# Kernel tuning notes

Measured on AMD Instinct MI355X. Metric: run time of the kernel, lower is better.

Reference implementation:

```python
import jax, jax.numpy as jnp
import numpy as np

TEAM = 5
N_PLAYER = 131072
PD = 256
HD = 256
MLP_H = 512
B = 16384

def _combine(t=TEAM):
    i1, i2 = [], []
    for i in range(t):
        for j in range(t):
            if i != j:
                i1.append(i); i2.append(j)
    return np.array(i1), np.array(i2)

IDX1, IDX2 = _combine()

def setup_inputs() -> dict:
    key = jax.random.key(0)
    ks = jax.random.split(key, 12)
    def xavier(k, shape):
        fan_in, fan_out = shape[1], shape[0]
        std = np.sqrt(2.0 / (fan_in + fan_out))
        return (jax.random.normal(k, shape, dtype=jnp.float32) * std)
    return {
        'team_ids': jax.random.randint(ks[0], (B, TEAM), 0, N_PLAYER),
        'emb': xavier(ks[1], (N_PLAYER, PD)),
        'fm_w1': xavier(ks[2], (2 * HD, PD)),
        'fm_b1': jnp.zeros((2 * HD,), jnp.float32),
        'fm_w2': xavier(ks[3], (HD, 2 * HD)),
        'fm_b2': jnp.zeros((HD,), jnp.float32),
        'att_w': xavier(ks[4], (HD, HD)),
        'att_b': jnp.zeros((HD,), jnp.float32),
        'mlp_w1': xavier(ks[5], (MLP_H, HD)),
        'mlp_b1': jnp.zeros((MLP_H,), jnp.float32),
        'mlp_w2': xavier(ks[6], (1, MLP_H)),
        'mlp_b2': jnp.zeros((1,), jnp.float32),
    }

def reference(team_ids, emb, fm_w1, fm_b1, fm_w2, fm_b2, att_w, att_b,
              mlp_w1, mlp_b1, mlp_w2, mlp_b2):
    # embedding lookup: [B, 5, PD]
    x = emb[team_ids]
    # feature mapper: Linear -> SiLU -> Linear  => [B, 5, HD]
    h = jax.nn.silu(jnp.einsum('btp,hp->bth', x, fm_w1) + fm_b1)
    h = jnp.einsum('bth,oh->bto', h, fm_w2) + fm_b2
    # pairwise gather (20 ordered pairs): [B, 20, HD]
    a = h[:, IDX1]
    b = h[:, IDX2]
    prod = a * b
    # small MLP (dropout is inference identity): [B, 20]
    m = jax.nn.silu(jnp.einsum('bph,mh->bpm', prod, mlp_w1) + mlp_b1)
    order2 = (jnp.einsum('bpm,om->bpo', m, mlp_w2) + mlp_b2)[..., 0]
    # attention (reduce=True -> view [B, 5, 4, HD], softmax over axis 2)
    wa = jnp.einsum('bph,oh->bpo', a, att_w) + att_b
    score = (wa * b).sum(-1).reshape(-1, TEAM, TEAM - 1)
    normal = jax.nn.softmax(score, axis=2).reshape(-1, TEAM * (TEAM - 1))
    order2 = order2 * normal
    return order2.sum(axis=1, keepdims=True)  # [B, 1]
```

## Files before the change

### kernel.cpp

```cpp
#include <hip/hip_runtime.h>

#define NB     16384
#define TEAM   5
#define NPAIR  20
#define UPAIR  10
#define PD     256
#define HD     256
#define H1D    512
#define NPLAY  (NB*TEAM)
#define NCHUNK 1

typedef __attribute__((ext_vector_type(4))) float f32x4;
typedef __attribute__((ext_vector_type(8))) short s16x8;

__device__ __forceinline__ float silu_f(float x){ return x / (1.0f + __expf(-x)); }

__device__ __forceinline__ unsigned short bf16_rne(float x){
  unsigned u = __float_as_uint(x);
  unsigned r = u + 0x7fffu + ((u >> 16) & 1u);
  return (unsigned short)(r >> 16);
}
__device__ __forceinline__ float bf16_to_f(unsigned short s){
  return __uint_as_float(((unsigned)s) << 16);
}
__device__ __forceinline__ void tsplit(float x, short& h, short& l){
  const unsigned u = __float_as_uint(x);
  h = (short)(u >> 16);
  const float lf = x - __uint_as_float(u & 0xffff0000u);
  l = (short)(__float_as_uint(lf) >> 16);
}

__global__ void k_pack(const float* __restrict__ w, short* __restrict__ wf,
                       int KT, int total)
{
  const int tid = blockIdx.x * 256 + threadIdx.x;
  if (tid >= total) return;
  const int slot = tid & 7;
  const int lane = (tid >> 3) & 63;
  const int grp  = tid >> 9;
  const int kt   = grp % KT;
  const int nt   = grp / KT;
  const int K    = KT * 32;
  const int n = nt * 16 + (lane & 15);
  const int k = kt * 32 + ((lane >> 4) << 3) + slot;
  const float v = w[(size_t)n * K + k];
  const unsigned short hi = bf16_rne(v);
  const float lo = v - bf16_to_f(hi);
  wf[tid]         = (short)hi;
  wf[total + tid] = (short)bf16_rne(lo);
}

__global__ __launch_bounds__(256) void k_l1(
    const int* __restrict__ tids, const float* __restrict__ emb,
    const short* __restrict__ w1f, const float* __restrict__ b1,
    float* __restrict__ Hh1)
{
  __shared__ short Af[10240];
  __shared__ float Bb[256];
  __shared__ int   Tid[80];

  const int t = threadIdx.x, lane = t & 63, w = t >> 6;
  const int bx = blockIdx.x, cy = blockIdx.y;
  const int p0 = bx * 80;

  if (t < 80) Tid[t] = tids[p0 + t];
  Bb[t] = b1[cy * 256 + t];

  f32x4 acc[5][4];
  #pragma unroll
  for (int mt = 0; mt < 5; ++mt)
    #pragma unroll
    for (int j = 0; j < 4; ++j) acc[mt][j] = (f32x4){0.f,0.f,0.f,0.f};

  const s16x8* Bh = reinterpret_cast<const s16x8*>(w1f);

  for (int kt = 0; kt < 8; ++kt) {
    const int kc = kt >> 1, ks = kt & 1;
    if (ks == 0) {
      __syncthreads();
      const int kt0 = kc * 64;
      #pragma unroll
      for (int f = 0; f < 5; ++f) {
        const int idx4  = t + f * 256;
        const int sg    = (idx4 & 1) * 4;
        const int lane_ = (idx4 >> 1) & 63;
        const int ks_   = (idx4 >> 7) & 1;
        const int mt_   = idx4 >> 8;
        const int p     = mt_ * 16 + (lane_ & 15);
        const int k     = kt0 + ks_ * 32 + ((lane_ >> 4) << 3) + sg;
        const int row   = Tid[p];
        const float4 a4 = *reinterpret_cast<const float4*>(emb + (size_t)row * PD + k);
        float pv[4] = {a4.x, a4.y, a4.z, a4.w};
        short hi[4], lo[4];
        #pragma unroll
        for (int e = 0; e < 4; ++e) tsplit(pv[e], hi[e], lo[e]);
        const int aoff = (mt_ * 2 + ks_) * 512 + lane_ * 8 + sg;
        *reinterpret_cast<short4*>(&Af[aoff])        = make_short4(hi[0],hi[1],hi[2],hi[3]);
        *reinterpret_cast<short4*>(&Af[5120 + aoff]) = make_short4(lo[0],lo[1],lo[2],lo[3]);
      }
      __syncthreads();
    }

    s16x8 ah[5], al[5];
    #pragma unroll
    for (int mt = 0; mt < 5; ++mt) {
      ah[mt] = *reinterpret_cast<const s16x8*>(&Af[(mt*2 + ks)*512 + lane*8]);
      al[mt] = *reinterpret_cast<const s16x8*>(&Af[5120 + (mt*2 + ks)*512 + lane*8]);
    }
    #pragma unroll
    for (int j = 0; j < 4; ++j) {
      const int nt = cy * 16 + w * 4 + j;
      const s16x8 bh = Bh[(nt*8 + kt)*64 + lane];
      const s16x8 bl = Bh[16384 + (nt*8 + kt)*64 + lane];
      #pragma unroll
      for (int mt = 0; mt < 5; ++mt) {
        acc[mt][j] = __builtin_amdgcn_mfma_f32_16x16x32_bf16(ah[mt], bh, acc[mt][j], 0,0,0);
        acc[mt][j] = __builtin_amdgcn_mfma_f32_16x16x32_bf16(al[mt], bh, acc[mt][j], 0,0,0);
        acc[mt][j] = __builtin_amdgcn_mfma_f32_16x16x32_bf16(ah[mt], bl, acc[mt][j], 0,0,0);
      }
    }
  }

  #pragma unroll
  for (int mt = 0; mt < 5; ++mt)
    #pragma unroll
    for (int j = 0; j < 4; ++j) {
      const int nl = w * 64 + j * 16 + (lane & 15);
      const int n  = cy * 256 + nl;
      #pragma unroll
      for (int r = 0; r < 4; ++r) {
        const int p = p0 + mt*16 + ((lane >> 4) << 2) + r;
        Hh1[(size_t)p * H1D + n] = silu_f(acc[mt][j][r] + Bb[nl]);
      }
    }
}

__global__ __launch_bounds__(256) void k_l2(
    const float* __restrict__ Hh1, const short* __restrict__ w2f,
    const float* __restrict__ b2, float* __restrict__ Hout)
{
  __shared__ short Af[10240];
  __shared__ float Bb[256];

  const int t = threadIdx.x, lane = t & 63, w = t >> 6;
  const int bx = blockIdx.x;
  const int p0 = bx * 80;

  Bb[t] = b2[t];

  const int sg    = (t & 1) * 4;
  const int lane_ = (t >> 1) & 63;
  const int ks_   = (t >> 7) & 1;
  const int kb    = ks_ * 32 + ((lane_ >> 4) << 3) + sg;
  int rowH[5], aof[5];
  #pragma unroll
  for (int f = 0; f < 5; ++f) {
    rowH[f] = (p0 + f * 16 + (lane_ & 15)) * H1D;
    aof[f]  = (f * 2 + ks_) * 512 + lane_ * 8 + sg;
  }

  f32x4 acc[5][4];
  #pragma unroll
  for (int mt = 0; mt < 5; ++mt)
    #pragma unroll
    for (int j = 0; j < 4; ++j) acc[mt][j] = (f32x4){0.f,0.f,0.f,0.f};

  const s16x8* B2 = reinterpret_cast<const s16x8*>(w2f);

  for (int kt = 0; kt < 16; ++kt) {
    const int kc = kt >> 1, ks = kt & 1;
    if (ks == 0) {
      __syncthreads();
      const int kk = kc * 64 + kb;
      #pragma unroll
      for (int f = 0; f < 5; ++f) {
        const float4 a4 = *reinterpret_cast<const float4*>(Hh1 + rowH[f] + kk);
        float pv[4] = {a4.x, a4.y, a4.z, a4.w};
        short hi[4], lo[4];
        #pragma unroll
        for (int e = 0; e < 4; ++e) tsplit(pv[e], hi[e], lo[e]);
        *reinterpret_cast<short4*>(&Af[aof[f]])        = make_short4(hi[0],hi[1],hi[2],hi[3]);
        *reinterpret_cast<short4*>(&Af[5120 + aof[f]]) = make_short4(lo[0],lo[1],lo[2],lo[3]);
      }
      __syncthreads();
    }

    s16x8 ah[5], al[5];
    #pragma unroll
    for (int mt = 0; mt < 5; ++mt) {
      ah[mt] = *reinterpret_cast<const s16x8*>(&Af[(mt*2 + ks)*512 + lane*8]);
      al[mt] = *reinterpret_cast<const s16x8*>(&Af[5120 + (mt*2 + ks)*512 + lane*8]);
    }
    #pragma unroll
    for (int j = 0; j < 4; ++j) {
      const int nt = w * 4 + j;
      const s16x8 bh = B2[(nt*16 + kt)*64 + lane];
      const s16x8 bl = B2[16384 + (nt*16 + kt)*64 + lane];
      #pragma unroll
      for (int mt = 0; mt < 5; ++mt) {
        acc[mt][j] = __builtin_amdgcn_mfma_f32_16x16x32_bf16(ah[mt], bh, acc[mt][j], 0,0,0);
        acc[mt][j] = __builtin_amdgcn_mfma_f32_16x16x32_bf16(al[mt], bh, acc[mt][j], 0,0,0);
        acc[mt][j] = __builtin_amdgcn_mfma_f32_16x16x32_bf16(ah[mt], bl, acc[mt][j], 0,0,0);
      }
    }
  }

  #pragma unroll
  for (int mt = 0; mt < 5; ++mt)
    #pragma unroll
    for (int j = 0; j < 4; ++j) {
      const int n = w * 64 + j * 16 + (lane & 15);
      #pragma unroll
      for (int r = 0; r < 4; ++r) {
        const int p = p0 + mt*16 + ((lane >> 4) << 2) + r;
        Hout[(size_t)p * PD + n] = acc[mt][j][r] + Bb[n];
      }
    }
}

__global__ __launch_bounds__(256) void k_fm4(
    const int* __restrict__ tids, const float* __restrict__ emb,
    const short* __restrict__ w1f, const float* __restrict__ b1,
    const short* __restrict__ w2f, const float* __restrict__ b2,
    float* __restrict__ Hout)
{
  __shared__ char smem[65536 + 3072];
  short* Af  = reinterpret_cast<short*>(smem);
  short* H1f = reinterpret_cast<short*>(smem);
  float* Bb  = reinterpret_cast<float*>(smem + 65536);

  const int t = threadIdx.x, lane = t & 63, w = t >> 6;
  const int m0 = blockIdx.x * 32;

  Bb[t]       = b1[t];
  Bb[t + 256] = b1[t + 256];
  Bb[t + 512] = b2[t];

  #pragma unroll
  for (int f = 0; f < 8; ++f) {
    const int g     = t + f * 256;
    const int sg    = (g & 1) * 4;
    const int lane_ = (g >> 1) & 63;
    const int kt_   = (g >> 7) & 7;
    const int mt_   = g >> 10;
    const int p     = mt_ * 16 + (lane_ & 15);
    const int k     = kt_ * 32 + ((lane_ >> 4) << 3) + sg;
    const int row   = tids[m0 + p];
    const float4 a4 = *reinterpret_cast<const float4*>(emb + (size_t)row * PD + k);
    float pv[4] = {a4.x, a4.y, a4.z, a4.w};
    short hi[4], lo[4];
    #pragma unroll
    for (int e = 0; e < 4; ++e) {
      const unsigned short h = bf16_rne(pv[e]);
      hi[e] = (short)h;
      lo[e] = (short)bf16_rne(pv[e] - bf16_to_f(h));
    }
    const int off = ((mt_*8 + kt_)*64 + lane_)*8 + sg;
    *reinterpret_cast<short4*>(&Af[off])        = make_short4(hi[0],hi[1],hi[2],hi[3]);
    *reinterpret_cast<short4*>(&Af[8192 + off]) = make_short4(lo[0],lo[1],lo[2],lo[3]);
  }
  __syncthreads();

  const s16x8* B1 = reinterpret_cast<const s16x8*>(w1f);
  const s16x8* B2 = reinterpret_cast<const s16x8*>(w2f);

  f32x4 acc1[2][8];
  #pragma unroll
  for (int mt = 0; mt < 2; ++mt)
    #pragma unroll
    for (int j = 0; j < 8; ++j) acc1[mt][j] = (f32x4){0.f,0.f,0.f,0.f};

  #pragma unroll
  for (int kt = 0; kt < 8; ++kt) {
    s16x8 ah[2], al[2];
    #pragma unroll
    for (int mt = 0; mt < 2; ++mt) {
      ah[mt] = *reinterpret_cast<const s16x8*>(&Af[((mt*8 + kt)*64 + lane)*8]);
      al[mt] = *reinterpret_cast<const s16x8*>(&Af[8192 + ((mt*8 + kt)*64 + lane)*8]);
    }
    #pragma unroll
    for (int j = 0; j < 8; ++j) {
      const int nt = w * 8 + j;
      const s16x8 bh = B1[(nt*8 + kt)*64 + lane];
      const s16x8 bl = B1[16384 + (nt*8 + kt)*64 + lane];
      #pragma unroll
      for (int mt = 0; mt < 2; ++mt) {
        acc1[mt][j] = __builtin_amdgcn_mfma_f32_16x16x32_bf16(ah[mt], bh, acc1[mt][j], 0,0,0);
        acc1[mt][j] = __builtin_amdgcn_mfma_f32_16x16x32_bf16(al[mt], bh, acc1[mt][j], 0,0,0);
        acc1[mt][j] = __builtin_amdgcn_mfma_f32_16x16x32_bf16(ah[mt], bl, acc1[mt][j], 0,0,0);
      }
    }
  }
  __syncthreads();

  #pragma unroll
  for (int mt = 0; mt < 2; ++mt)
    #pragma unroll
    for (int j = 0; j < 8; ++j) {
      const int n     = w * 128 + j * 16 + (lane & 15);
      const int kt2   = n >> 5;
      const int lhalf = 16 * ((n >> 3) & 3);
      const int slot2 = n & 7;
      #pragma unroll
      for (int r = 0; r < 4; ++r) {
        const int prow = ((lane >> 4) << 2) + r;
        const float v = silu_f(acc1[mt][j][r] + Bb[n]);
        const unsigned short hi = bf16_rne(v);
        const int off = ((mt*16 + kt2)*64 + lhalf + prow)*8 + slot2;
        H1f[off]         = (short)hi;
        H1f[16384 + off] = (short)bf16_rne(v - bf16_to_f(hi));
      }
    }
  __syncthreads();

  f32x4 acc2[2][4];
  #pragma unroll
  for (int mt = 0; mt < 2; ++mt)
    #pragma unroll
    for (int j = 0; j < 4; ++j) acc2[mt][j] = (f32x4){0.f,0.f,0.f,0.f};

  #pragma unroll
  for (int kt = 0; kt < 16; ++kt) {
    s16x8 ah[2], al[2];
    #pragma unroll
    for (int mt = 0; mt < 2; ++mt) {
      ah[mt] = *reinterpret_cast<const s16x8*>(&H1f[((mt*16 + kt)*64 + lane)*8]);
      al[mt] = *reinterpret_cast<const s16x8*>(&H1f[16384 + ((mt*16 + kt)*64 + lane)*8]);
    }
    #pragma unroll
    for (int j = 0; j < 4; ++j) {
      const int nt = w * 4 + j;
      const s16x8 bh = B2[(nt*16 + kt)*64 + lane];
      const s16x8 bl = B2[16384 + (nt*16 + kt)*64 + lane];
      #pragma unroll
      for (int mt = 0; mt < 2; ++mt) {
        acc2[mt][j] = __builtin_amdgcn_mfma_f32_16x16x32_bf16(ah[mt], bh, acc2[mt][j], 0,0,0);
        acc2[mt][j] = __builtin_amdgcn_mfma_f32_16x16x32_bf16(al[mt], bh, acc2[mt][j], 0,0,0);
        acc2[mt][j] = __builtin_amdgcn_mfma_f32_16x16x32_bf16(ah[mt], bl, acc2[mt][j], 0,0,0);
      }
    }
  }

  #pragma unroll
  for (int mt = 0; mt < 2; ++mt)
    #pragma unroll
    for (int j = 0; j < 4; ++j) {
      const int n = w * 64 + j * 16 + (lane & 15);
      #pragma unroll
      for (int r = 0; r < 4; ++r) {
        const int p = m0 + mt*16 + ((lane >> 4) << 2) + r;
        Hout[(size_t)p * PD + n] = acc2[mt][j][r] + Bb[512 + n];
      }
    }
}

__global__ __launch_bounds__(256) void k_score(
    const float* __restrict__ Hin, const short* __restrict__ attf,
    const float* __restrict__ attb, float* __restrict__ SC)
{
  __shared__ char smem[49152 + 1024];
  short* Hf  = reinterpret_cast<short*>(smem);
  float* WAl = reinterpret_cast<float*>(smem);
  float* Ab  = reinterpret_cast<float*>(smem + 49152);

  const int t = threadIdx.x, lane = t & 63, w = t >> 6;
  const int b0 = blockIdx.x * 8;
  const float* src = Hin + (size_t)b0 * TEAM * PD;

  Ab[t] = attb[t];

  #pragma unroll
  for (int f = 0; f < 12; ++f) {
    const int g     = t + f * 256;
    const int sg    = (g & 1) * 4;
    const int lane_ = (g >> 1) & 63;
    const int kt_   = (g >> 7) & 7;
    const int mt_   = g >> 10;
    const int p     = mt_ * 16 + (lane_ & 15);
    const int k     = kt_ * 32 + ((lane_ >> 4) << 3) + sg;
    float4 a4 = make_float4(0.f, 0.f, 0.f, 0.f);
    if (p < 40) a4 = *reinterpret_cast<const float4*>(src + (size_t)p * PD + k);
    float pv[4] = {a4.x, a4.y, a4.z, a4.w};
    short hi[4], lo[4];
    #pragma unroll
    for (int e = 0; e < 4; ++e) tsplit(pv[e], hi[e], lo[e]);
    const int off = ((mt_*8 + kt_)*64 + lane_)*8 + sg;
    *reinterpret_cast<short4*>(&Hf[off])         = make_short4(hi[0],hi[1],hi[2],hi[3]);
    *reinterpret_cast<short4*>(&Hf[12288 + off]) = make_short4(lo[0],lo[1],lo[2],lo[3]);
  }
  __syncthreads();

  f32x4 acc[3][4];
  #pragma unroll
  for (int mt = 0; mt < 3; ++mt)
    #pragma unroll
    for (int j = 0; j < 4; ++j) acc[mt][j] = (f32x4){0.f,0.f,0.f,0.f};

  const s16x8* Bh = reinterpret_cast<const s16x8*>(attf);
  #pragma unroll
  for (int kt = 0; kt < 8; ++kt) {
    s16x8 ah[3], al[3];
    #pragma unroll
    for (int mt = 0; mt < 3; ++mt) {
      ah[mt] = *reinterpret_cast<const s16x8*>(&Hf[((mt*8 + kt)*64 + lane)*8]);
      al[mt] = *reinterpret_cast<const s16x8*>(&Hf[12288 + ((mt*8 + kt)*64 + lane)*8]);
    }
    #pragma unroll
    for (int j = 0; j < 4; ++j) {
      const int nt = w * 4 + j;
      const s16x8 bh = Bh[(nt*8 + kt)*64 + lane];
      const s16x8 bl = Bh[8192 + (nt*8 + kt)*64 + lane];
      #pragma unroll
      for (int mt = 0; mt < 3; ++mt) {
        acc[mt][j] = __builtin_amdgcn_mfma_f32_16x16x32_bf16(ah[mt], bh, acc[mt][j], 0,0,0);
        acc[mt][j] = __builtin_amdgcn_mfma_f32_16x16x32_bf16(al[mt], bh, acc[mt][j], 0,0,0);
        acc[mt][j] = __builtin_amdgcn_mfma_f32_16x16x32_bf16(ah[mt], bl, acc[mt][j], 0,0,0);
      }
    }
  }
  __syncthreads();

  #pragma unroll
  for (int mt = 0; mt < 3; ++mt)
    #pragma unroll
    for (int j = 0; j < 4; ++j) {
      const int n = w * 64 + j * 16 + (lane & 15);
      #pragma unroll
      for (int r = 0; r < 4; ++r) {
        const int row = mt * 16 + ((lane >> 4) << 2) + r;
        if (row < 40) WAl[row * 260 + n] = acc[mt][j][r] + Ab[n];
      }
    }
  __syncthreads();

  #pragma unroll
  for (int qq = 0; qq < 2; ++qq) {
    const int q = w * 2 + qq;
    #pragma unroll
    for (int p = 0; p < NPAIR; ++p) {
      const int i1 = p >> 2, jj = p & 3;
      const int i2 = jj + (jj >= i1 ? 1 : 0);
      const float4 a4 = *reinterpret_cast<const float4*>(WAl + (q*TEAM + i1) * 260 + lane * 4);
      const float4 b4 = *reinterpret_cast<const float4*>(src + (size_t)(q*TEAM + i2) * PD + lane * 4);
      float v = a4.x*b4.x + a4.y*b4.y + a4.z*b4.z + a4.w*b4.w;
      #pragma unroll
      for (int off = 32; off > 0; off >>= 1) v += __shfl_xor(v, off);
      if (lane == 0) SC[(size_t)(b0 + q) * NPAIR + p] = v;
    }
  }
}

__global__ __launch_bounds__(512, 4) void k_mlp(
    const float* __restrict__ Hin, const short* __restrict__ w1f,
    const float* __restrict__ b1, const float* __restrict__ w2,
    float* __restrict__ PART)
{
  __shared__ float Hl[40*260];
  __shared__ short Af[10240];
  __shared__ float Wb[512];
  __shared__ float Ww[512];
  __shared__ float red[640];

  const int t    = threadIdx.x;
  const int lane = t & 63;
  const int w    = t >> 6;
  const int blkx = blockIdx.x;
  const int b0   = blkx * 8;
  const float* src = Hin + (size_t)b0 * TEAM * PD;

  {
    #pragma unroll
    for (int rep = 0; rep < 5; ++rep) {
      const int flat = t + rep * 512;
      const int row = flat >> 6, c4 = (flat & 63) * 4;
      *reinterpret_cast<float4*>(Hl + row * 260 + c4) =
        *reinterpret_cast<const float4*>(src + (size_t)row * PD + c4);
    }
    Wb[t] = b1[t];
    Ww[t] = w2[t];
  }

  f32x4 acc[5][4];
  #pragma unroll
  for (int mt = 0; mt < 5; ++mt)
    #pragma unroll
    for (int j = 0; j < 4; ++j) acc[mt][j] = (f32x4){0.f,0.f,0.f,0.f};

  const s16x8* Bh = reinterpret_cast<const s16x8*>(w1f);
  const s16x8* Bl = reinterpret_cast<const s16x8*>(w1f + 131072);
  const int nt0 = w * 4;

  for (int kt = 0; kt < 8; ++kt) {
    const int kc = kt >> 1, ks = kt & 1;
    if (ks == 0) {
      __syncthreads();
      const int kt0 = kc * 64;
      #pragma unroll
      for (int f = 0; f < 3; ++f) {
        const int idx4 = t + f * 512;
        if (idx4 < 1280) {
          const int sg    = (idx4 & 1) * 4;
          const int lane_ = (idx4 >> 1) & 63;
          const int ks_   = (idx4 >> 7) & 1;
          const int mt_   = idx4 >> 8;
          const int r  = mt_ * 16 + (lane_ & 15);
          const int q  = r / UPAIR;
          const int p  = r - q * UPAIR;
          const int i1 = (p >= 4) + (p >= 7) + (p >= 9);
          const int i2 = p - (i1 * (9 - i1)) / 2 + i1 + 1;
          const int kk = kt0 + ks_ * 32 + ((lane_ >> 4) << 3) + sg;
          const float4 a4 = *reinterpret_cast<const float4*>(Hl + (q*TEAM + i1)*260 + kk);
          const float4 b4 = *reinterpret_cast<const float4*>(Hl + (q*TEAM + i2)*260 + kk);
          float pv[4] = {a4.x*b4.x, a4.y*b4.y, a4.z*b4.z, a4.w*b4.w};
          short hi[4], lo[4];
          #pragma unroll
          for (int e = 0; e < 4; ++e) tsplit(pv[e], hi[e], lo[e]);
          const int aoff = (mt_ * 2 + ks_) * 512 + lane_ * 8 + sg;
          *reinterpret_cast<short4*>(&Af[aoff])        = make_short4(hi[0],hi[1],hi[2],hi[3]);
          *reinterpret_cast<short4*>(&Af[5120 + aoff]) = make_short4(lo[0],lo[1],lo[2],lo[3]);
        }
      }
      __syncthreads();
    }

    s16x8 ah[5], al[5];
    #pragma unroll
    for (int mt = 0; mt < 5; ++mt) {
      ah[mt] = *reinterpret_cast<const s16x8*>(&Af[(mt*2 + ks)*512 + lane*8]);
      al[mt] = *reinterpret_cast<const s16x8*>(&Af[5120 + (mt*2 + ks)*512 + lane*8]);
    }
    #pragma unroll
    for (int j = 0; j < 4; ++j) {
      const s16x8 bh = Bh[((nt0 + j)*8 + kt)*64 + lane];
      const s16x8 bl = Bl[((nt0 + j)*8 + kt)*64 + lane];
      #pragma unroll
      for (int mt = 0; mt < 5; ++mt) {
        acc[mt][j] = __builtin_amdgcn_mfma_f32_16x16x32_bf16(ah[mt], bh, acc[mt][j], 0,0,0);
        acc[mt][j] = __builtin_amdgcn_mfma_f32_16x16x32_bf16(ah[mt], bl, acc[mt][j], 0,0,0);
        acc[mt][j] = __builtin_amdgcn_mfma_f32_16x16x32_bf16(al[mt], bh, acc[mt][j], 0,0,0);
      }
    }
  }

  __syncthreads();

  const int colbase = w * 64 + (lane & 15);
  #pragma unroll
  for (int mt = 0; mt < 5; ++mt)
    #pragma unroll
    for (int r = 0; r < 4; ++r) {
      float s = 0.0f;
      #pragma unroll
      for (int j = 0; j < 4; ++j) {
        const int c = colbase + j * 16;
        s += silu_f(acc[mt][j][r] + Wb[c]) * Ww[c];
      }
      s += __shfl_xor(s, 1); s += __shfl_xor(s, 2);
      s += __shfl_xor(s, 4); s += __shfl_xor(s, 8);
      if ((lane & 15) == 0) {
        const int row = mt * 16 + ((lane >> 4) << 2) + r;
        red[row * 8 + w] = s;
      }
    }
  __syncthreads();
  if (t < 80) {
    float s = 0.0f;
    #pragma unroll
    for (int g = 0; g < 8; ++g) s += red[t*8 + g];
    PART[(size_t)blkx * 80 + t] = s;
  }
}

__global__ void k_final(const float* __restrict__ SC, const float* __restrict__ PART,
                        const float* __restrict__ mb2, float* __restrict__ out)
{
  const int b = blockIdx.x * 256 + threadIdx.x;
  if (b >= NB) return;
  const float bias2 = mb2[0];
  float ord[UPAIR];
  #pragma unroll
  for (int u = 0; u < UPAIR; ++u) {
    float s = bias2;
    #pragma unroll
    for (int g = 0; g < NCHUNK; ++g) s += PART[(size_t)g * (NB*UPAIR) + (size_t)b * UPAIR + u];
    ord[u] = s;
  }
  float sc[NPAIR];
  #pragma unroll
  for (int p = 0; p < NPAIR; ++p) sc[p] = SC[(size_t)b * NPAIR + p];

  float res = 0.0f;
  #pragma unroll
  for (int i = 0; i < TEAM; ++i) {
    float m = sc[4*i];
    #pragma unroll
    for (int jj = 1; jj < 4; ++jj) m = fmaxf(m, sc[4*i + jj]);
    float e[4], d = 0.0f;
    #pragma unroll
    for (int jj = 0; jj < 4; ++jj) { e[jj] = __expf(sc[4*i + jj] - m); d += e[jj]; }
    const float inv = 1.0f / d;
    #pragma unroll
    for (int jj = 0; jj < 4; ++jj) {
      const int i2 = jj + (jj >= i ? 1 : 0);
      const int a  = i < i2 ? i : i2;
      const int bb = i < i2 ? i2 : i;
      const int u  = (a * (9 - a)) / 2 + (bb - a - 1);
      res += ord[u] * e[jj] * inv;
    }
  }
  out[b] = res;
}

extern "C" void kernel_launch(void* const* d_in, const int* in_sizes, int n_in,
                              void* d_out, int out_size, void* d_ws, size_t ws_size,
                              hipStream_t stream)
{
  (void)in_sizes; (void)n_in; (void)out_size;
  const int*   tids = (const int*)  d_in[0];
  const float* emb  = (const float*)d_in[1];
  const float* fw1  = (const float*)d_in[2];
  const float* fb1  = (const float*)d_in[3];
  const float* fw2  = (const float*)d_in[4];
  const float* fb2  = (const float*)d_in[5];
  const float* attw = (const float*)d_in[6];
  const float* attb = (const float*)d_in[7];
  const float* mw1  = (const float*)d_in[8];
  const float* mb1  = (const float*)d_in[9];
  const float* mw2  = (const float*)d_in[10];
  const float* mb2  = (const float*)d_in[11];
  float* out = (float*)d_out;

  float* H     = (float*)d_ws;
  float* SC    = H + (size_t)NPLAY * PD;
  float* PART  = SC + (size_t)NB * NPAIR;
  short* w1f_m = (short*)(PART + (size_t)NCHUNK * NB * UPAIR);
  short* w1f_f = w1f_m + 262144;
  short* w2f_f = w1f_f + 262144;
  short* attf  = w2f_f + 262144;
  float* Hh1   = (float*)(attf + 131072);
  const size_t NEED = (size_t)((char*)(Hh1 + (size_t)NPLAY * H1D) - (char*)d_ws);

  k_pack<<<512, 256, 0, stream>>>(mw1, w1f_m, 8, 131072);
  k_pack<<<512, 256, 0, stream>>>(fw1, w1f_f, 8, 131072);
  k_pack<<<512, 256, 0, stream>>>(fw2, w2f_f, 16, 131072);
  k_pack<<<256, 256, 0, stream>>>(attw, attf, 8, 65536);

  if (ws_size >= NEED) {
    k_l1<<<dim3(NPLAY/80, 2), 256, 0, stream>>>(tids, emb, w1f_f, fb1, Hh1);
    k_l2<<<NPLAY/80, 256, 0, stream>>>(Hh1, w2f_f, fb2, H);
  } else {
    k_fm4<<<NPLAY/32, 256, 0, stream>>>(tids, emb, w1f_f, fb1, w2f_f, fb2, H);
  }
  k_score<<<NB/8, 256, 0, stream>>>(H, attf, attb, SC);
  k_mlp<<<NB/8, 512, 0, stream>>>(H, w1f_m, mb1, mw2, PART);
  k_final<<<NB/256, 256, 0, stream>>>(SC, PART, mb2, out);
}
```

Before: 744.3 us.

## Halve k_mlp block to 256 threads with 8 N-tiles per wave

The MLP kernel now runs with 4 waves instead of 8, and each wave covers 128 output columns (8 N-tiles) instead of 64. Each A fragment loaded from LDS is therefore reused across twice as many MFMAs. Per-thread pair row offsets are precomputed once outside the k loop, and the reduction buffer reuses the Af shared array, which lowers LDS use. In exchange each thread holds twice as many accumulators (160 floats), which raises register pressure and may cut occupancy or cause spills.

```diff
diff --git a/kernel.cpp b/kernel.cpp
--- a/kernel.cpp
+++ b/kernel.cpp
@@ -450,7 +450,7 @@
   }
 }
 
-__global__ __launch_bounds__(512, 4) void k_mlp(
+__global__ __launch_bounds__(256, 2) void k_mlp(
     const float* __restrict__ Hin, const short* __restrict__ w1f,
     const float* __restrict__ b1, const float* __restrict__ w2,
     float* __restrict__ PART)
@@ -459,7 +459,6 @@
   __shared__ short Af[10240];
   __shared__ float Wb[512];
   __shared__ float Ww[512];
-  __shared__ float red[640];
 
   const int t    = threadIdx.x;
   const int lane = t & 63;
@@ -470,55 +469,60 @@
 
   {
     #pragma unroll
-    for (int rep = 0; rep < 5; ++rep) {
-      const int flat = t + rep * 512;
+    for (int rep = 0; rep < 10; ++rep) {
+      const int flat = t + rep * 256;
       const int row = flat >> 6, c4 = (flat & 63) * 4;
       *reinterpret_cast<float4*>(Hl + row * 260 + c4) =
         *reinterpret_cast<const float4*>(src + (size_t)row * PD + c4);
     }
-    Wb[t] = b1[t];
-    Ww[t] = w2[t];
-  }
-
-  f32x4 acc[5][4];
+    Wb[t]       = b1[t];
+    Wb[t + 256] = b1[t + 256];
+    Ww[t]       = w2[t];
+    Ww[t + 256] = w2[t + 256];
+  }
+
+  const int sg    = (t & 1) * 4;
+  const int lane_ = (t >> 1) & 63;
+  const int ks_   = (t >> 7) & 1;
+  const int kb    = ks_ * 32 + ((lane_ >> 4) << 3) + sg;
+  int rowA[5], rowB[5], aof[5];
+  #pragma unroll
+  for (int f = 0; f < 5; ++f) {
+    const int r  = f * 16 + (lane_ & 15);
+    const int q  = r / UPAIR;
+    const int p  = r - q * UPAIR;
+    const int i1 = (p >= 4) + (p >= 7) + (p >= 9);
+    const int i2 = p - (i1 * (9 - i1)) / 2 + i1 + 1;
+    rowA[f] = (q * TEAM + i1) * 260;
+    rowB[f] = (q * TEAM + i2) * 260;
+    aof[f]  = (f * 2 + ks_) * 512 + lane_ * 8 + sg;
+  }
+
+  f32x4 acc[5][8];
   #pragma unroll
   for (int mt = 0; mt < 5; ++mt)
     #pragma unroll
-    for (int j = 0; j < 4; ++j) acc[mt][j] = (f32x4){0.f,0.f,0.f,0.f};
+    for (int j = 0; j < 8; ++j) acc[mt][j] = (f32x4){0.f,0.f,0.f,0.f};
 
   const s16x8* Bh = reinterpret_cast<const s16x8*>(w1f);
   const s16x8* Bl = reinterpret_cast<const s16x8*>(w1f + 131072);
-  const int nt0 = w * 4;
+  const int nt0 = w * 8;
 
   for (int kt = 0; kt < 8; ++kt) {
     const int kc = kt >> 1, ks = kt & 1;
     if (ks == 0) {
       __syncthreads();
-      const int kt0 = kc * 64;
-      #pragma unroll
-      for (int f = 0; f < 3; ++f) {
-        const int idx4 = t + f * 512;
-        if (idx4 < 1280) {
-          const int sg    = (idx4 & 1) * 4;
-          const int lane_ = (idx4 >> 1) & 63;
-          const int ks_   = (idx4 >> 7) & 1;
-          const int mt_   = idx4 >> 8;
-          const int r  = mt_ * 16 + (lane_ & 15);
-          const int q  = r / UPAIR;
-          const int p  = r - q * UPAIR;
-          const int i1 = (p >= 4) + (p >= 7) + (p >= 9);
-          const int i2 = p - (i1 * (9 - i1)) / 2 + i1 + 1;
-          const int kk = kt0 + ks_ * 32 + ((lane_ >> 4) << 3) + sg;
-          const float4 a4 = *reinterpret_cast<const float4*>(Hl + (q*TEAM + i1)*260 + kk);
-          const float4 b4 = *reinterpret_cast<const float4*>(Hl + (q*TEAM + i2)*260 + kk);
-          float pv[4] = {a4.x*b4.x, a4.y*b4.y, a4.z*b4.z, a4.w*b4.w};
-          short hi[4], lo[4];
-          #pragma unroll
-          for (int e = 0; e < 4; ++e) tsplit(pv[e], hi[e], lo[e]);
-          const int aoff = (mt_ * 2 + ks_) * 512 + lane_ * 8 + sg;
-          *reinterpret_cast<short4*>(&Af[aoff])        = make_short4(hi[0],hi[1],hi[2],hi[3]);
-          *reinterpret_cast<short4*>(&Af[5120 + aoff]) = make_short4(lo[0],lo[1],lo[2],lo[3]);
-        }
+      const int kk = kc * 64 + kb;
+      #pragma unroll
+      for (int f = 0; f < 5; ++f) {
+        const float4 a4 = *reinterpret_cast<const float4*>(Hl + rowA[f] + kk);
+        const float4 b4 = *reinterpret_cast<const float4*>(Hl + rowB[f] + kk);
+        float pv[4] = {a4.x*b4.x, a4.y*b4.y, a4.z*b4.z, a4.w*b4.w};
+        short hi[4], lo[4];
+        #pragma unroll
+        for (int e = 0; e < 4; ++e) tsplit(pv[e], hi[e], lo[e]);
+        *reinterpret_cast<short4*>(&Af[aof[f]])        = make_short4(hi[0],hi[1],hi[2],hi[3]);
+        *reinterpret_cast<short4*>(&Af[5120 + aof[f]]) = make_short4(lo[0],lo[1],lo[2],lo[3]);
       }
       __syncthreads();
     }
@@ -530,7 +534,7 @@
       al[mt] = *reinterpret_cast<const s16x8*>(&Af[5120 + (mt*2 + ks)*512 + lane*8]);
     }
     #pragma unroll
-    for (int j = 0; j < 4; ++j) {
+    for (int j = 0; j < 8; ++j) {
       const s16x8 bh = Bh[((nt0 + j)*8 + kt)*64 + lane];
       const s16x8 bl = Bl[((nt0 + j)*8 + kt)*64 + lane];
       #pragma unroll
@@ -543,15 +547,16 @@
   }
 
   __syncthreads();
-
-  const int colbase = w * 64 + (lane & 15);
+  float* red = reinterpret_cast<float*>(Af);
+
+  const int colbase = w * 128 + (lane & 15);
   #pragma unroll
   for (int mt = 0; mt < 5; ++mt)
     #pragma unroll
     for (int r = 0; r < 4; ++r) {
       float s = 0.0f;
       #pragma unroll
-      for (int j = 0; j < 4; ++j) {
+      for (int j = 0; j < 8; ++j) {
         const int c = colbase + j * 16;
         s += silu_f(acc[mt][j][r] + Wb[c]) * Ww[c];
       }
@@ -559,14 +564,12 @@
       s += __shfl_xor(s, 4); s += __shfl_xor(s, 8);
       if ((lane & 15) == 0) {
         const int row = mt * 16 + ((lane >> 4) << 2) + r;
-        red[row * 8 + w] = s;
+        red[row * 4 + w] = s;
       }
     }
   __syncthreads();
   if (t < 80) {
-    float s = 0.0f;
-    #pragma unroll
-    for (int g = 0; g < 8; ++g) s += red[t*8 + g];
+    const float s = red[t*4] + red[t*4+1] + red[t*4+2] + red[t*4+3];
     PART[(size_t)blkx * 80 + t] = s;
   }
 }
@@ -652,6 +655,6 @@
     k_fm4<<<NPLAY/32, 256, 0, stream>>>(tids, emb, w1f_f, fb1, w2f_f, fb2, H);
   }
   k_score<<<NB/8, 256, 0, stream>>>(H, attf, attb, SC);
-  k_mlp<<<NB/8, 512, 0, stream>>>(H, w1f_m, mb1, mw2, PART);
+  k_mlp<<<NB/8, 256, 0, stream>>>(H, w1f_m, mb1, mw2, PART);
   k_final<<<NB/256, 256, 0, stream>>>(SC, PART, mb2, out);
 }
```

After: 602.0 us. 1.24x faster.
